# Kernel optimization log

Measured on AMD Instinct MI355X. Metric: run time of the kernel, lower is better.

Reference implementation:

```python
import jax, jax.numpy as jnp
import numpy as np

N_POINTS = 4096
DIM = 64
MAX_EDGE_LENGTH = 1e9  # large -> no MST edge is filtered, output has static shape (n-1,)


def _mst_edge_lengths(points):
    """0-dim Rips persistence death values == Euclidean MST edge lengths.

    Equivalent to gudhi RipsComplex(max_dimension=0) + flag_persistence_generators
    followed by torch.norm(input[v0] - input[v1], dim=-1). Returned sorted
    ascending (gudhi's ordering is unspecified; compare as a multiset).
    """
    n = points.shape[0]
    sq = jnp.sum(points * points, axis=1)                      # [n]
    d2 = sq[:, None] + sq[None, :] - 2.0 * (points @ points.T)  # [n,n]
    d2 = jnp.maximum(d2, 0.0)
    # safe positive diagonal so sqrt is smooth there (diagonal never selected)
    idx = jnp.arange(n)
    d2 = d2.at[idx, idx].set(1.0)
    D = jnp.sqrt(d2)                                            # [n,n] distances

    inf = jnp.asarray(jnp.inf, D.dtype)
    in_tree0 = jnp.zeros((n,), dtype=bool).at[0].set(True)
    dist0 = jnp.where(in_tree0, inf, D[0])                      # min dist to tree

    def step(carry, _):
        dist, in_tree = carry
        j = jnp.argmin(dist)            # nearest non-tree vertex
        w = dist[j]                     # MST edge length (a persistence death)
        in_tree = in_tree.at[j].set(True)
        dist = jnp.where(in_tree, inf, jnp.minimum(dist, D[j]))
        return (dist, in_tree), w

    _, lengths = jax.lax.scan(step, (dist0, in_tree0), None, length=n - 1)
    # max_edge_length filter is a no-op for MAX_EDGE_LENGTH=1e9
    return jnp.sort(lengths)


def setup_inputs() -> dict:
    key = jax.random.key(0)
    points = jax.random.normal(key, (N_POINTS, DIM), dtype=jnp.float32)
    return {"input": points}


def reference(input) -> jnp.ndarray:
    return _mst_edge_lengths(input)
```

## Files before the change

kernel.cpp:

```cpp
#include <hip/hip_runtime.h>
#include <hip/hip_bf16.h>


#define NPTS 4096
#define SENT 1e30f
#define KINF 0xFFFFFFFFFFFFFFFFull
#define INV32 0xFFFFFFFFu
#define SCAN_ROWS 2
#define SCAN_BLOCKS (NPTS / SCAN_ROWS)
#define CMAX 1024

#define HOOK_NORMAL 0
#define HOOK_FORCE_COMPACT 1

typedef short short8 __attribute__((ext_vector_type(8)));
typedef float f32x4 __attribute__((ext_vector_type(4)));

__device__ __forceinline__ float bfbits2f(unsigned int u16) {
  union { unsigned int u; float f; } c;
  c.u = u16 << 16;
  return c.f;
}

__device__ bool data_is_bf16(const unsigned short* p) {
  bool bf = true;
  for (int i = 0; i < 256; ++i) {
    float f = bfbits2f((unsigned int)p[i]);
    if (!(f > -1e6f && f < 1e6f)) bf = false;
  }
  return bf;
}

__global__ __launch_bounds__(256) void prep_kernel(
    const void* pts_raw, unsigned short* Pb, float* sq, int* comp,
    unsigned short* comp16, int* parent, unsigned long long* cheapest,
    float* edges, unsigned* cnt, unsigned* M) {
  float pf = bfbits2f((unsigned int)((const unsigned short*)pts_raw)[threadIdx.x]);
  const bool bfs = (bool)__syncthreads_and((int)(pf > -1e6f && pf < 1e6f));

  const int g = blockIdx.x * 256 + threadIdx.x;
  if (g < NPTS) {
    comp[g] = g;
    comp16[g] = (unsigned short)g;
    parent[g] = g;
    cheapest[g] = KINF;
  }
  {
    uint4 mi; mi.x = INV32; mi.y = INV32; mi.z = INV32; mi.w = INV32;
    ((uint4*)M)[g] = mi;
  }
  if (g == NPTS - 1) edges[NPTS - 1] = SENT;
  if (g == 0) {
    cnt[0] = 0u;
    cnt[1] = 0u;
    cnt[2] = bfs ? 1u : 0u;
    cnt[3] = 0u;
  }

  const int row = g >> 6;
  const int lane = threadIdx.x & 63;

  unsigned short ub;
  if (bfs) {
    ub = ((const unsigned short*)pts_raw)[row * 64 + lane];
  } else {
    __hip_bfloat16 h = __float2bfloat16(((const float*)pts_raw)[row * 64 + lane]);
    ub = *(unsigned short*)&h;
  }
  Pb[row * 64 + lane] = ub;

  float v = bfbits2f((unsigned int)ub);
  float s = v * v;
#pragma unroll
  for (int m = 1; m < 64; m <<= 1) s += __shfl_xor(s, m);
  if (lane == 0) sq[row] = s;
}

__global__ __launch_bounds__(256) void dist_mfma(const unsigned short* Pb,
                                                 const float* sq,
                                                 unsigned short* Dbf,
                                                 unsigned long long* cheapest) {
  __shared__ unsigned short tile[64 * 72];

  const int t = threadIdx.x;
  const int w = t >> 6, lane = t & 63;
  const int quad = lane >> 4, l16 = lane & 15;
  const int rbase = blockIdx.y * 64 + w * 16;
  const int cbase = blockIdx.x * 64;

  const short8* Pv = (const short8*)Pb;
  short8 a0 = Pv[(rbase + l16) * 8 + quad];
  short8 a1 = Pv[(rbase + l16) * 8 + quad + 4];

  f32x4 acc[4];
#pragma unroll
  for (int c = 0; c < 4; ++c) {
    short8 b0 = Pv[(cbase + c * 16 + l16) * 8 + quad];
    short8 b1 = Pv[(cbase + c * 16 + l16) * 8 + quad + 4];
    f32x4 z = {0.f, 0.f, 0.f, 0.f};
    z = __builtin_amdgcn_mfma_f32_16x16x32_bf16(a0, b0, z, 0, 0, 0);
    z = __builtin_amdgcn_mfma_f32_16x16x32_bf16(a1, b1, z, 0, 0, 0);
    acc[c] = z;
  }

  float sr[4];
#pragma unroll
  for (int q = 0; q < 4; ++q) sr[q] = sq[rbase + quad * 4 + q];

#pragma unroll
  for (int c = 0; c < 4; ++c) {
    float sc = sq[cbase + c * 16 + l16];
#pragma unroll
    for (int q = 0; q < 4; ++q) {
      float d2 = sr[q] + sc - 2.f * acc[c][q];
      float dd = sqrtf(fmaxf(d2, 0.f));
      __hip_bfloat16 h = __float2bfloat16(dd);
      tile[(w * 16 + quad * 4 + q) * 72 + c * 16 + l16] = *(unsigned short*)&h;
    }
  }
  __syncthreads();

  for (int i = t; i < 512; i += 256) {
    int row = i >> 3, cb8 = (i & 7) * 8;
    uint4 v = *(const uint4*)&tile[row * 72 + cb8];
    *(uint4*)&Dbf[(size_t)(blockIdx.y * 64 + row) * 4096 + cbase + cb8] = v;
  }

  {
    const int r = t >> 2, cseg = (t & 3) * 16;
    const int v = blockIdx.y * 64 + r;
    const uint4* lrow = (const uint4*)&tile[r * 72 + cseg];
    uint4 v0 = lrow[0], v1 = lrow[1];
    unsigned wv[16] = {v0.x & 0xFFFFu, v0.x >> 16, v0.y & 0xFFFFu, v0.y >> 16,
                       v0.z & 0xFFFFu, v0.z >> 16, v0.w & 0xFFFFu, v0.w >> 16,
                       v1.x & 0xFFFFu, v1.x >> 16, v1.y & 0xFFFFu, v1.y >> 16,
                       v1.z & 0xFFFFu, v1.z >> 16, v1.w & 0xFFFFu, v1.w >> 16};
    unsigned long long kmin = KINF;
#pragma unroll
    for (int e = 0; e < 16; ++e) {
      const int j = cbase + cseg + e;
      if (j != v) {
        unsigned ed = (v < j) ? (((unsigned)v << 12) | (unsigned)j)
                              : (((unsigned)j << 12) | (unsigned)v);
        unsigned long long key = ((unsigned long long)wv[e] << 24) | ed;
        kmin = key < kmin ? key : kmin;
      }
    }
#pragma unroll
    for (int m = 1; m < 4; m <<= 1) {
      unsigned long long o = __shfl_xor(kmin, m);
      kmin = o < kmin ? o : kmin;
    }
    if ((t & 3) == 0) atomicMin(&cheapest[v], kmin);
  }
}

__global__ __launch_bounds__(256) void bor_scan(const unsigned short* Dbf,
                                                const unsigned short* comp16,
                                                int* parent,
                                                unsigned long long* cheapest,
                                                const unsigned* cnt) {
  if (cnt[1]) return;

  __shared__ unsigned long long redu[SCAN_ROWS][4];

  const int t = threadIdx.x;
  const int b = blockIdx.x;
  const int wave = t >> 6;
  const int gtid = b * 256 + t;
  const int vbase = b * SCAN_ROWS;

  if (gtid < NPTS) parent[gtid] = gtid;

  const uint4* c16v = (const uint4*)comp16;
  uint4 c0 = c16v[2 * t], c1 = c16v[2 * t + 1];
  unsigned mc[16] = {c0.x & 0xFFFFu, c0.x >> 16, c0.y & 0xFFFFu, c0.y >> 16,
                     c0.z & 0xFFFFu, c0.z >> 16, c0.w & 0xFFFFu, c0.w >> 16,
                     c1.x & 0xFFFFu, c1.x >> 16, c1.y & 0xFFFFu, c1.y >> 16,
                     c1.z & 0xFFFFu, c1.z >> 16, c1.w & 0xFFFFu, c1.w >> 16};

  const uint4* rp = (const uint4*)(Dbf + (size_t)vbase * NPTS);
#pragma unroll
  for (int vv = 0; vv < SCAN_ROWS; ++vv) {
    const int v = vbase + vv;
    const unsigned cv = (unsigned)comp16[v];
    uint4 a0 = rp[vv * 512 + 2 * t];
    uint4 a1 = rp[vv * 512 + 2 * t + 1];
    unsigned wv[16] = {a0.x & 0xFFFFu, a0.x >> 16, a0.y & 0xFFFFu, a0.y >> 16,
                       a0.z & 0xFFFFu, a0.z >> 16, a0.w & 0xFFFFu, a0.w >> 16,
                       a1.x & 0xFFFFu, a1.x >> 16, a1.y & 0xFFFFu, a1.y >> 16,
                       a1.z & 0xFFFFu, a1.z >> 16, a1.w & 0xFFFFu, a1.w >> 16};
    unsigned long long kmin = KINF;
#pragma unroll
    for (int e = 0; e < 16; ++e) {
      const int j = t * 16 + e;
      if (mc[e] != cv) {
        unsigned ed = (v < j) ? (((unsigned)v << 12) | (unsigned)j)
                              : (((unsigned)j << 12) | (unsigned)v);
        unsigned long long key = ((unsigned long long)wv[e] << 24) | ed;
        kmin = key < kmin ? key : kmin;
      }
    }
#pragma unroll
    for (int m = 1; m < 64; m <<= 1) {
      unsigned long long o = __shfl_xor(kmin, m);
      kmin = o < kmin ? o : kmin;
    }
    if ((t & 63) == 0) redu[vv][wave] = kmin;
  }
  __syncthreads();

  if (t < SCAN_ROWS) {
    unsigned long long k = redu[t][0];
    if (redu[t][1] < k) k = redu[t][1];
    if (redu[t][2] < k) k = redu[t][2];
    if (redu[t][3] < k) k = redu[t][3];
    if (k != KINF) atomicMin(&cheapest[(int)comp16[vbase + t]], k);
  }
}

__global__ __launch_bounds__(1024) void bor_hook(int* comp,
                                                 unsigned short* comp16,
                                                 int* parent,
                                                 unsigned long long* cheapest,
                                                 float* edges, unsigned* cnt,
                                                 int mode) {
  if (cnt[1]) return;
  const int t = threadIdx.x;

  for (int i = t; i < NPTS; i += 1024) {
    if (comp[i] == i) {
      unsigned long long key = cheapest[i];
      if (key != KINF) {
        int mx = (int)(key & 0xFFFull);
        int mn = (int)((key >> 12) & 0xFFFull);
        int ca = comp[mn], cb = comp[mx];
        int u = (ca == i) ? cb : ca;
        bool mutual = (cheapest[u] == key);
        if (!mutual || i < u) {
          unsigned pos = atomicAdd(cnt, 1u);
          edges[pos] = bfbits2f((unsigned)(key >> 24));
        }
        if (!mutual || i > u) parent[i] = u;
      }
    }
  }
  __threadfence_block();
  __syncthreads();

  for (int i = t; i < NPTS; i += 1024) {
    int r = comp[i], p;
    for (int it = 0; it < NPTS; ++it) {
      p = parent[r];
      if (p == r) break;
      r = p;
    }
    comp[i] = r;
    comp16[i] = (unsigned short)r;
    cheapest[i] = KINF;
  }
  __threadfence_block();
  __syncthreads();

  if (mode == HOOK_FORCE_COMPACT) {
    for (int i = t; i < NPTS; i += 1024)
      if (comp[i] == i) parent[i] = (int)atomicAdd(&cnt[3], 1u);
    __syncthreads();
    for (int i = t; i < NPTS; i += 1024)
      comp16[i] = (unsigned short)parent[comp[i]];
  }
  if (t == 0 && cnt[0] >= (unsigned)(NPTS - 1)) cnt[1] = 1u;
}

__global__ __launch_bounds__(256) void bor_project(const unsigned short* Dbf,
                                                   const unsigned short* comp16,
                                                   unsigned* M,
                                                   const unsigned* cnt) {
  if (cnt[1]) return;

  __shared__ unsigned Mloc[SCAN_ROWS][CMAX];
  const int t = threadIdx.x;
  const int b = blockIdx.x;
  const int vbase = b * SCAN_ROWS;

#pragma unroll
  for (int s = 0; s < 4; ++s) {
    Mloc[0][t + 256 * s] = INV32;
    Mloc[1][t + 256 * s] = INV32;
  }
  __syncthreads();

  const uint4* c16v = (const uint4*)comp16;
  uint4 c0 = c16v[2 * t], c1 = c16v[2 * t + 1];
  unsigned mc[16] = {c0.x & 0xFFFFu, c0.x >> 16, c0.y & 0xFFFFu, c0.y >> 16,
                     c0.z & 0xFFFFu, c0.z >> 16, c0.w & 0xFFFFu, c0.w >> 16,
                     c1.x & 0xFFFFu, c1.x >> 16, c1.y & 0xFFFFu, c1.y >> 16,
                     c1.z & 0xFFFFu, c1.z >> 16, c1.w & 0xFFFFu, c1.w >> 16};

  const uint4* rp = (const uint4*)(Dbf + (size_t)vbase * NPTS);
#pragma unroll
  for (int vv = 0; vv < SCAN_ROWS; ++vv) {
    const unsigned cv = (unsigned)comp16[vbase + vv];
    uint4 a0 = rp[vv * 512 + 2 * t];
    uint4 a1 = rp[vv * 512 + 2 * t + 1];
    unsigned wv[16] = {a0.x & 0xFFFFu, a0.x >> 16, a0.y & 0xFFFFu, a0.y >> 16,
                       a0.z & 0xFFFFu, a0.z >> 16, a0.w & 0xFFFFu, a0.w >> 16,
                       a1.x & 0xFFFFu, a1.x >> 16, a1.y & 0xFFFFu, a1.y >> 16,
                       a1.z & 0xFFFFu, a1.z >> 16, a1.w & 0xFFFFu, a1.w >> 16};
#pragma unroll
    for (int e = 0; e < 16; ++e)
      if (mc[e] != cv) atomicMin(&Mloc[vv][mc[e]], wv[e]);
  }
  __syncthreads();

  const unsigned cv0 = (unsigned)comp16[vbase];
  const unsigned cv1 = (unsigned)comp16[vbase + 1];
#pragma unroll
  for (int s = 0; s < 4; ++s) {
    const int col = t + 256 * s;
    unsigned x = Mloc[0][col];
    if (x != INV32) atomicMin(&M[cv0 * CMAX + col], x);
    unsigned y = Mloc[1][col];
    if (y != INV32) atomicMin(&M[cv1 * CMAX + col], y);
  }
}

__global__ __launch_bounds__(1024) void bor_finish(const unsigned* M,
                                                   unsigned* cnt,
                                                   float* edges) {
  if (cnt[1]) return;

  __shared__ int comp2[CMAX];
  __shared__ int parent2[CMAX];
  __shared__ unsigned long long cheap2[CMAX];
  __shared__ int live;

  const int t = threadIdx.x;
  const int C = (int)cnt[3];
  comp2[t] = t;
  __syncthreads();

  for (int round = 0; round < 11; ++round) {
    cheap2[t] = KINF;
    if (t == 0) live = 0;
    __syncthreads();

    {
      const int q = t & 1;
      for (int c = t >> 1; c < C; c += 512) {
        const int cc = comp2[c];
        unsigned long long kmin = KINF;
        const uint4* Mr = (const uint4*)(M + c * CMAX + q * 512);
#pragma unroll 4
        for (int g = 0; g < 128; ++g) {
          uint4 m4 = Mr[g];
          const int j0 = q * 512 + g * 4;
          unsigned wj[4] = {m4.x, m4.y, m4.z, m4.w};
#pragma unroll
          for (int k = 0; k < 4; ++k) {
            int j = j0 + k;
            unsigned w = wj[k];
            if (w != INV32 && comp2[j] != cc) {
              int lo = c < j ? c : j, hi = c < j ? j : c;
              unsigned long long key = ((unsigned long long)w << 22) |
                                       ((unsigned)lo << 11) | (unsigned)hi;
              if (key < kmin) kmin = key;
            }
          }
        }
        if (kmin != KINF) atomicMin(&cheap2[cc], kmin);
      }
    }
    __syncthreads();

    {
      parent2[t] = t;
      if (comp2[t] == t) {
        unsigned long long key = cheap2[t];
        if (key != KINF) {
          int hi = (int)(key & 0x7FFull);
          int lo = (int)((key >> 11) & 0x7FFull);
          int ca = comp2[lo], cb = comp2[hi];
          int u = (ca == t) ? cb : ca;
          bool mutual = (cheap2[u] == key);
          if (!mutual || t < u) {
            unsigned pos = atomicAdd(cnt, 1u);
            edges[pos] = bfbits2f((unsigned)(key >> 22));
          }
          if (!mutual || t > u) parent2[t] = u;
        }
      }
    }
    __syncthreads();

    {
      int r = comp2[t], p;
      for (int it = 0; it < CMAX; ++it) {
        p = parent2[r];
        if (p == r) break;
        r = p;
      }
      comp2[t] = r;
      if (t < C && r != comp2[0]) live = 1;
    }
    __syncthreads();
    if (!live) break;
  }
}

__global__ __launch_bounds__(256) void rank_sort(const float* edges,
                                                 const unsigned* cnt,
                                                 void* out) {
  __shared__ unsigned long long wred[4][2];
  const int b = blockIdx.x;
  const int t = threadIdx.x;
  const int pbase = 4 * b;
  const float4* ev = (const float4*)edges;
  const float4 pvv = ev[b];
  const float pv0 = pvv.x, pv1 = pvv.y, pv2 = pvv.z, pv3 = pvv.w;

  int c0 = 0, c1 = 0, c2 = 0, c3 = 0;
#pragma unroll
  for (int k = 0; k < 4; ++k) {
    float4 e = ev[t + 256 * k];
    int j = 4 * (t + 256 * k);
    float va[4] = {e.x, e.y, e.z, e.w};
#pragma unroll
    for (int m = 0; m < 4; ++m) {
      const float x = va[m];
      const int xi = j + m;
      c0 += (x < pv0 || (x == pv0 && xi < pbase + 0));
      c1 += (x < pv1 || (x == pv1 && xi < pbase + 1));
      c2 += (x < pv2 || (x == pv2 && xi < pbase + 2));
      c3 += (x < pv3 || (x == pv3 && xi < pbase + 3));
    }
  }

  unsigned long long p0 = (unsigned long long)(unsigned)c0 |
                          ((unsigned long long)(unsigned)c1 << 32);
  unsigned long long p1 = (unsigned long long)(unsigned)c2 |
                          ((unsigned long long)(unsigned)c3 << 32);
#pragma unroll
  for (int m = 1; m < 64; m <<= 1) {
    p0 += __shfl_xor(p0, m);
    p1 += __shfl_xor(p1, m);
  }
  if ((t & 63) == 0) { wred[t >> 6][0] = p0; wred[t >> 6][1] = p1; }
  __syncthreads();

  if (t == 0) {
    unsigned long long a = wred[0][0] + wred[1][0] + wred[2][0] + wred[3][0];
    unsigned long long d = wred[0][1] + wred[1][1] + wred[2][1] + wred[3][1];
    const int r[4] = {(int)(a & 0xFFFFFFFFull), (int)(a >> 32),
                      (int)(d & 0xFFFFFFFFull), (int)(d >> 32)};
    const float pv[4] = {pv0, pv1, pv2, pv3};
    const bool bf = cnt[2] != 0u;
#pragma unroll
    for (int p = 0; p < 4; ++p) {
      const int pidx = pbase + p;
      if (pidx < NPTS - 1) {
        if (bf) ((__hip_bfloat16*)out)[r[p]] = __float2bfloat16(pv[p]);
        else    ((float*)out)[r[p]] = pv[p];
      }
    }
  }
}

__global__ __launch_bounds__(256) void dist_kernel(const void* pts_raw,
                                                   __hip_bfloat16* Dbf) {
  __shared__ float As[64 * 65];
  __shared__ float Bs[64 * 65];
  __shared__ float sqA[64];
  __shared__ float sqB[64];

  const int t = threadIdx.x;
  const int bx = blockIdx.x, by = blockIdx.y;
  const bool bf = data_is_bf16((const unsigned short*)pts_raw);
  const unsigned short* pu = (const unsigned short*)pts_raw;
  const float* pf = (const float*)pts_raw;

  for (int s = 0; s < 16; ++s) {
    int e = t + 256 * s;
    int r = e >> 6, c = e & 63;
    float av, bv;
    if (bf) {
      av = bfbits2f((unsigned int)pu[by * 4096 + e]);
      bv = bfbits2f((unsigned int)pu[bx * 4096 + e]);
    } else {
      av = pf[by * 4096 + e];
      bv = pf[bx * 4096 + e];
    }
    As[r * 65 + c] = av;
    Bs[r * 65 + c] = bv;
  }
  __syncthreads();

  if (t < 64) {
    float s = 0.f;
    for (int k = 0; k < 64; ++k) { float x = As[t * 65 + k]; s += x * x; }
    sqA[t] = s;
  } else if (t < 128) {
    int r = t - 64;
    float s = 0.f;
    for (int k = 0; k < 64; ++k) { float x = Bs[r * 65 + k]; s += x * x; }
    sqB[r] = s;
  }
  __syncthreads();

  const int tx = t & 15, ty = t >> 4;
  const int lr = ty * 4, lc = tx * 4;
  float acc[4][4] = {};
  for (int k = 0; k < 64; ++k) {
    float a[4], b[4];
#pragma unroll
    for (int q = 0; q < 4; ++q) a[q] = As[(lr + q) * 65 + k];
#pragma unroll
    for (int p = 0; p < 4; ++p) b[p] = Bs[(lc + p) * 65 + k];
#pragma unroll
    for (int q = 0; q < 4; ++q)
#pragma unroll
      for (int p = 0; p < 4; ++p) acc[q][p] += a[q] * b[p];
  }

#pragma unroll
  for (int q = 0; q < 4; ++q) {
    int gr = by * 64 + lr + q;
    float sa = sqA[lr + q];
#pragma unroll
    for (int p = 0; p < 4; ++p) {
      int gc = bx * 64 + lc + p;
      float d2 = sa + sqB[lc + p] - 2.f * acc[q][p];
      d2 = fmaxf(d2, 0.f);
      Dbf[(size_t)gr * 4096 + gc] = __float2bfloat16(sqrtf(d2));
    }
  }
}

__global__ __launch_bounds__(512) void prim_kernel(const unsigned short* probe,
                                                   const unsigned short* Dbf,
                                                   void* out) {
  __shared__ float len[NPTS];
  __shared__ float rv[2][8];
  __shared__ int ri[2][8];

  const int t = threadIdx.x;
  const bool bf_out = data_is_bf16(probe);

  float d[8];
  {
    const uint4* row0 = (const uint4*)(Dbf);
    uint4 v = row0[t];
    d[0] = bfbits2f(v.x & 0xffffu); d[1] = bfbits2f(v.x >> 16);
    d[2] = bfbits2f(v.y & 0xffffu); d[3] = bfbits2f(v.y >> 16);
    d[4] = bfbits2f(v.z & 0xffffu); d[5] = bfbits2f(v.z >> 16);
    d[6] = bfbits2f(v.w & 0xffffu); d[7] = bfbits2f(v.w >> 16);
    if (t == 0) d[0] = SENT;
  }

  float bv = SENT;
  int bi = 8 * t;
#pragma unroll
  for (int k = 0; k < 8; ++k)
    if (d[k] < bv) { bv = d[k]; bi = 8 * t + k; }

  for (int step = 0; step < NPTS - 1; ++step) {
    float v = bv;
    int idx = bi;
#pragma unroll
    for (int m = 1; m < 64; m <<= 1) {
      float ov = __shfl_xor(v, m);
      int oi = __shfl_xor(idx, m);
      if (ov < v) { v = ov; idx = oi; }
    }
    const int buf = step & 1;
    if ((t & 63) == 0) { rv[buf][t >> 6] = v; ri[buf][t >> 6] = idx; }
    __syncthreads();

    float w = rv[buf][0];
    int j = ri[buf][0];
#pragma unroll
    for (int u = 1; u < 8; ++u) {
      float uv = rv[buf][u];
      if (uv < w) { w = uv; j = ri[buf][u]; }
    }
    if (t == 0) len[step] = w;

    const uint4* row = (const uint4*)(Dbf + (size_t)j * NPTS);
    uint4 rw = row[t];
    float nd[8];
    nd[0] = bfbits2f(rw.x & 0xffffu); nd[1] = bfbits2f(rw.x >> 16);
    nd[2] = bfbits2f(rw.y & 0xffffu); nd[3] = bfbits2f(rw.y >> 16);
    nd[4] = bfbits2f(rw.z & 0xffffu); nd[5] = bfbits2f(rw.z >> 16);
    nd[6] = bfbits2f(rw.w & 0xffffu); nd[7] = bfbits2f(rw.w >> 16);

    bv = SENT;
    bi = 8 * t;
    const int base = 8 * t;
#pragma unroll
    for (int k = 0; k < 8; ++k) {
      float cur = d[k];
      float nn = fminf(cur, nd[k]);
      if (cur == SENT || base + k == j) nn = SENT;
      d[k] = nn;
      if (nn < bv) { bv = nn; bi = base + k; }
    }
  }

  if (t == 0) len[NPTS - 1] = SENT;
  __syncthreads();

  for (int k = 2; k <= NPTS; k <<= 1) {
    for (int jj = k >> 1; jj > 0; jj >>= 1) {
      for (int i = t; i < NPTS; i += 512) {
        int ixj = i ^ jj;
        if (ixj > i) {
          float a = len[i], b = len[ixj];
          bool up = ((i & k) == 0);
          if ((a > b) == up) { len[i] = b; len[ixj] = a; }
        }
      }
      __syncthreads();
    }
  }

  if (bf_out) {
    __hip_bfloat16* o = (__hip_bfloat16*)out;
    for (int i = t; i < NPTS - 1; i += 512) o[i] = __float2bfloat16(len[i]);
  } else {
    float* o = (float*)out;
    for (int i = t; i < NPTS - 1; i += 512) o[i] = len[i];
  }
}

extern "C" void kernel_launch(void* const* d_in, const int* in_sizes, int n_in,
                              void* d_out, int out_size, void* d_ws, size_t ws_size,
                              hipStream_t stream) {
  const void* pts = d_in[0];
  char* base = (char*)d_ws;
  __hip_bfloat16* Dbf = (__hip_bfloat16*)base;

  size_t off = 32ull << 20;
  int* comp = (int*)(base + off);                  off += (size_t)NPTS * 4;
  int* parent = (int*)(base + off);                off += (size_t)NPTS * 4;
  unsigned long long* cheapest =
      (unsigned long long*)(base + off);           off += (size_t)NPTS * 8;
  float* edges = (float*)(base + off);             off += (size_t)NPTS * 4;
  unsigned* cnt = (unsigned*)(base + off);         off += 256;
  unsigned short* Pb = (unsigned short*)(base + off); off += (size_t)NPTS * 64 * 2;
  float* sq = (float*)(base + off);                off += (size_t)NPTS * 4;
  unsigned short* comp16 = (unsigned short*)(base + off); off += (size_t)NPTS * 2;
  unsigned* M = (unsigned*)(base + off);           off += (size_t)CMAX * CMAX * 4;

  if (ws_size >= off) {
    prep_kernel<<<1024, 256, 0, stream>>>(pts, Pb, sq, comp, comp16, parent,
                                          cheapest, edges, cnt, M);
    const unsigned short* Dus = (const unsigned short*)Dbf;
    dist_mfma<<<dim3(64, 64), 256, 0, stream>>>(Pb, sq, (unsigned short*)Dbf,
                                                cheapest);
    bor_hook<<<1, 1024, 0, stream>>>(comp, comp16, parent, cheapest, edges,
                                     cnt, HOOK_NORMAL);
    bor_scan<<<SCAN_BLOCKS, 256, 0, stream>>>(Dus, comp16, parent, cheapest,
                                              cnt);
    bor_hook<<<1, 1024, 0, stream>>>(comp, comp16, parent, cheapest, edges,
                                     cnt, HOOK_FORCE_COMPACT);
    bor_project<<<SCAN_BLOCKS, 256, 0, stream>>>(Dus, comp16, M, cnt);
    bor_finish<<<1, 1024, 0, stream>>>(M, cnt, edges);
    rank_sort<<<NPTS / 4, 256, 0, stream>>>(edges, cnt, d_out);
  } else {
    dist_kernel<<<dim3(64, 64), 256, 0, stream>>>(pts, Dbf);
    prim_kernel<<<1, 512, 0, stream>>>((const unsigned short*)pts,
                                       (const unsigned short*)Dbf, d_out);
  }
}
```

Before: 189.7 us.

## Fuse first-round cheapest-edge reduction into projection and rebalance finish scan

bor_project now also computes, per row component, the minimum packed (weight, lo, hi) edge key with a wave shuffle and block reduction, and atomically publishes it to a new cheapM array. bor_finish takes its first Boruvka round directly from cheapM instead of scanning the full CMAX x CMAX matrix. Later rounds split each component row into four chunks bounded by the live component count C rather than always two halves of 1024. This removes the first-round matrix scan in the single-block kernel and trims work past C, at the cost of extra reductions and 64-bit atomics in the projection kernel.

```diff
diff --git a/kernel.cpp b/kernel.cpp
--- a/kernel.cpp
+++ b/kernel.cpp
@@ -34,7 +34,7 @@
 __global__ __launch_bounds__(256) void prep_kernel(
     const void* pts_raw, unsigned short* Pb, float* sq, int* comp,
     unsigned short* comp16, int* parent, unsigned long long* cheapest,
-    float* edges, unsigned* cnt, unsigned* M) {
+    float* edges, unsigned* cnt, unsigned* M, unsigned long long* cheapM) {
   float pf = bfbits2f((unsigned int)((const unsigned short*)pts_raw)[threadIdx.x]);
   const bool bfs = (bool)__syncthreads_and((int)(pf > -1e6f && pf < 1e6f));
 
@@ -45,6 +45,7 @@
     parent[g] = g;
     cheapest[g] = KINF;
   }
+  if (g < CMAX) cheapM[g] = KINF;
   {
     uint4 mi; mi.x = INV32; mi.y = INV32; mi.z = INV32; mi.w = INV32;
     ((uint4*)M)[g] = mi;
@@ -275,10 +276,12 @@
 __global__ __launch_bounds__(256) void bor_project(const unsigned short* Dbf,
                                                    const unsigned short* comp16,
                                                    unsigned* M,
-                                                   const unsigned* cnt) {
+                                                   const unsigned* cnt,
+                                                   unsigned long long* cheapM) {
   if (cnt[1]) return;
 
   __shared__ unsigned Mloc[SCAN_ROWS][CMAX];
+  __shared__ unsigned long long redc[SCAN_ROWS][4];
   const int t = threadIdx.x;
   const int b = blockIdx.x;
   const int vbase = b * SCAN_ROWS;
@@ -315,19 +318,51 @@
 
   const unsigned cv0 = (unsigned)comp16[vbase];
   const unsigned cv1 = (unsigned)comp16[vbase + 1];
+  unsigned long long k0 = KINF, k1 = KINF;
 #pragma unroll
   for (int s = 0; s < 4; ++s) {
-    const int col = t + 256 * s;
+    const unsigned col = (unsigned)(t + 256 * s);
     unsigned x = Mloc[0][col];
-    if (x != INV32) atomicMin(&M[cv0 * CMAX + col], x);
+    if (x != INV32) {
+      atomicMin(&M[cv0 * CMAX + col], x);
+      unsigned lo = cv0 < col ? cv0 : col, hi = cv0 < col ? col : cv0;
+      unsigned long long key =
+          ((unsigned long long)x << 22) | (lo << 11) | hi;
+      if (key < k0) k0 = key;
+    }
     unsigned y = Mloc[1][col];
-    if (y != INV32) atomicMin(&M[cv1 * CMAX + col], y);
+    if (y != INV32) {
+      atomicMin(&M[cv1 * CMAX + col], y);
+      unsigned lo = cv1 < col ? cv1 : col, hi = cv1 < col ? col : cv1;
+      unsigned long long key =
+          ((unsigned long long)y << 22) | (lo << 11) | hi;
+      if (key < k1) k1 = key;
+    }
+  }
+
+#pragma unroll
+  for (int m = 1; m < 64; m <<= 1) {
+    unsigned long long o0 = __shfl_xor(k0, m);
+    if (o0 < k0) k0 = o0;
+    unsigned long long o1 = __shfl_xor(k1, m);
+    if (o1 < k1) k1 = o1;
+  }
+  if ((t & 63) == 0) { redc[0][t >> 6] = k0; redc[1][t >> 6] = k1; }
+  __syncthreads();
+  if (t < SCAN_ROWS) {
+    unsigned long long k = redc[t][0];
+    if (redc[t][1] < k) k = redc[t][1];
+    if (redc[t][2] < k) k = redc[t][2];
+    if (redc[t][3] < k) k = redc[t][3];
+    if (k != KINF)
+      atomicMin(&cheapM[(int)comp16[vbase + t]], k);
   }
 }
 
 __global__ __launch_bounds__(1024) void bor_finish(const unsigned* M,
                                                    unsigned* cnt,
-                                                   float* edges) {
+                                                   float* edges,
+                                                   const unsigned long long* cheapM) {
   if (cnt[1]) return;
 
   __shared__ int comp2[CMAX];
@@ -345,16 +380,21 @@
     if (t == 0) live = 0;
     __syncthreads();
 
-    {
-      const int q = t & 1;
-      for (int c = t >> 1; c < C; c += 512) {
+    if (round == 0) {
+      if (t < C) cheap2[t] = cheapM[t];
+    } else {
+      const int Cu4 = (C + 3) >> 2;
+      const int Q4 = (Cu4 + 3) >> 2;
+      for (int item = t; item < 4 * C; item += 1024) {
+        const int c = item >> 2, q = item & 3;
         const int cc = comp2[c];
+        const int lo4 = q * Q4;
+        int hi4 = lo4 + Q4; if (hi4 > Cu4) hi4 = Cu4;
         unsigned long long kmin = KINF;
-        const uint4* Mr = (const uint4*)(M + c * CMAX + q * 512);
-#pragma unroll 4
-        for (int g = 0; g < 128; ++g) {
-          uint4 m4 = Mr[g];
-          const int j0 = q * 512 + g * 4;
+        const uint4* Mr = (const uint4*)(M + c * CMAX);
+        for (int u = lo4; u < hi4; ++u) {
+          uint4 m4 = Mr[u];
+          const int j0 = u * 4;
           unsigned wj[4] = {m4.x, m4.y, m4.z, m4.w};
 #pragma unroll
           for (int k = 0; k < 4; ++k) {
@@ -650,10 +690,12 @@
   float* sq = (float*)(base + off);                off += (size_t)NPTS * 4;
   unsigned short* comp16 = (unsigned short*)(base + off); off += (size_t)NPTS * 2;
   unsigned* M = (unsigned*)(base + off);           off += (size_t)CMAX * CMAX * 4;
+  unsigned long long* cheapM =
+      (unsigned long long*)(base + off);           off += (size_t)CMAX * 8;
 
   if (ws_size >= off) {
     prep_kernel<<<1024, 256, 0, stream>>>(pts, Pb, sq, comp, comp16, parent,
-                                          cheapest, edges, cnt, M);
+                                          cheapest, edges, cnt, M, cheapM);
     const unsigned short* Dus = (const unsigned short*)Dbf;
     dist_mfma<<<dim3(64, 64), 256, 0, stream>>>(Pb, sq, (unsigned short*)Dbf,
                                                 cheapest);
@@ -663,8 +705,8 @@
                                               cnt);
     bor_hook<<<1, 1024, 0, stream>>>(comp, comp16, parent, cheapest, edges,
                                      cnt, HOOK_FORCE_COMPACT);
-    bor_project<<<SCAN_BLOCKS, 256, 0, stream>>>(Dus, comp16, M, cnt);
-    bor_finish<<<1, 1024, 0, stream>>>(M, cnt, edges);
+    bor_project<<<SCAN_BLOCKS, 256, 0, stream>>>(Dus, comp16, M, cnt, cheapM);
+    bor_finish<<<1, 1024, 0, stream>>>(M, cnt, edges, cheapM);
     rank_sort<<<NPTS / 4, 256, 0, stream>>>(edges, cnt, d_out);
   } else {
     dist_kernel<<<dim3(64, 64), 256, 0, stream>>>(pts, Dbf);
```

Result: faster. 164.5 us (-13.3%).
